# Performance work log

Measured on AMD Instinct MI355X. Metric: run time of the kernel, lower is better.

## Reference

```python
import jax, jax.numpy as jnp
import numpy as np

NUM_CLASSES = 1000
FEAT_DIM = 512
K = 2  # centers per class
BATCH = 32768


def setup_inputs() -> dict:
    key = jax.random.key(0)
    k1, k2, k3 = jax.random.split(key, 3)
    x = jax.random.normal(k1, (BATCH, FEAT_DIM), dtype=jnp.float32)
    labels = jax.random.randint(k2, (BATCH,), 0, NUM_CLASSES, dtype=jnp.int64)
    centers = jax.random.normal(k3, (NUM_CLASSES * K, FEAT_DIM), dtype=jnp.float32)
    return {"x": x, "labels": labels, "centers": centers}


def reference(x, labels, centers):
    # centers viewed as [num_classes, K, D]; gather per-sample class centers -> [B, K, D]
    c = centers.reshape(NUM_CLASSES, K, FEAT_DIM)[labels]
    # squared euclidean distance to each of the K centers, then min over K
    d = jnp.sum((x[:, None, :] - c) ** 2, axis=-1)  # [B, K]
    min_d = jnp.min(d, axis=-1)                      # [B]
    return jnp.mean(min_d)
```

## Files before the change

kernel.cpp:

```cpp
#include <hip/hip_runtime.h>

#define BATCH 32768
#define FEAT 512
#define KCENT 2

__global__ __launch_bounds__(256) void mcl_partial(
    const float* __restrict__ x,
    const int* __restrict__ labels,
    const float* __restrict__ centers,
    float* __restrict__ partial)
{
    const int wave = threadIdx.x >> 6;
    const int lane = threadIdx.x & 63;
    const int sample = blockIdx.x * 4 + wave;

    const int lab = labels[sample];
    const float* __restrict__ xrow = x + (size_t)sample * FEAT;
    const float* __restrict__ c0 = centers + (size_t)lab * (KCENT * FEAT);
    const float* __restrict__ c1 = c0 + FEAT;

    float d0 = 0.f, d1 = 0.f;
#pragma unroll
    for (int j = 0; j < 2; ++j) {
        const int off = j * 256 + lane * 4;
        const float4 xv = *(const float4*)(xrow + off);
        const float4 a  = *(const float4*)(c0 + off);
        const float4 b  = *(const float4*)(c1 + off);
        float e;
        e = xv.x - a.x; d0 += e * e;
        e = xv.y - a.y; d0 += e * e;
        e = xv.z - a.z; d0 += e * e;
        e = xv.w - a.w; d0 += e * e;
        e = xv.x - b.x; d1 += e * e;
        e = xv.y - b.y; d1 += e * e;
        e = xv.z - b.z; d1 += e * e;
        e = xv.w - b.w; d1 += e * e;
    }

#pragma unroll
    for (int s = 32; s > 0; s >>= 1) {
        d0 += __shfl_down(d0, s, 64);
        d1 += __shfl_down(d1, s, 64);
    }

    __shared__ float smin[4];
    if (lane == 0) smin[wave] = fminf(d0, d1);
    __syncthreads();
    if (threadIdx.x == 0)
        partial[blockIdx.x] = (smin[0] + smin[1]) + (smin[2] + smin[3]);
}

__global__ __launch_bounds__(256) void mcl_final(
    const float* __restrict__ partial, int n, float* __restrict__ out)
{
    float s = 0.f;
    for (int i = threadIdx.x; i < n; i += 256) s += partial[i];
#pragma unroll
    for (int sh = 32; sh > 0; sh >>= 1) s += __shfl_down(s, sh, 64);
    __shared__ float ws[4];
    const int wave = threadIdx.x >> 6;
    const int lane = threadIdx.x & 63;
    if (lane == 0) ws[wave] = s;
    __syncthreads();
    if (threadIdx.x == 0)
        out[0] = ((ws[0] + ws[1]) + (ws[2] + ws[3])) * (1.0f / (float)BATCH);
}

extern "C" void kernel_launch(void* const* d_in, const int* in_sizes, int n_in,
                              void* d_out, int out_size, void* d_ws, size_t ws_size,
                              hipStream_t stream) {
    const float* x       = (const float*)d_in[0];
    const int*   labels  = (const int*)d_in[1];
    const float* centers = (const float*)d_in[2];
    float* out = (float*)d_out;
    float* partial = (float*)d_ws;

    const int nblocks = BATCH / 4;
    mcl_partial<<<nblocks, 256, 0, stream>>>(x, labels, centers, partial);
    mcl_final<<<1, 256, 0, stream>>>(partial, nblocks, out);
}
```

Before: 108.2 us.

## Process four samples per wave with nontemporal x loads and fewer blocks

Each wave now handles four samples instead of one. Labels are loaded once per wave and broadcast by shuffle, the x rows are read with nontemporal loads, and the grid shrinks fourfold so the final reduction sums fewer partials with a compile-time trip count. The aim is to cut block launch and reduction overhead and keep the streamed x data from polluting cache used by the centers. In exchange, each wave serialises four reductions, which may lower memory-level parallelism unless the compiler overlaps the unrolled loads.

New measurement: 109.0 us. About the same (+0.8%).

```diff
diff --git a/kernel.cpp b/kernel.cpp
--- a/kernel.cpp
+++ b/kernel.cpp
@@ -3,6 +3,10 @@
 #define BATCH 32768
 #define FEAT 512
 #define KCENT 2
+#define SAMPLES_PER_WAVE 4
+#define NBLOCKS (BATCH / (4 * SAMPLES_PER_WAVE))
+
+typedef float vf4 __attribute__((ext_vector_type(4)));
 
 __global__ __launch_bounds__(256) void mcl_partial(
     const float* __restrict__ x,
@@ -12,49 +16,59 @@
 {
     const int wave = threadIdx.x >> 6;
     const int lane = threadIdx.x & 63;
-    const int sample = blockIdx.x * 4 + wave;
+    const int gw   = blockIdx.x * 4 + wave;
+    const int base = gw * SAMPLES_PER_WAVE;
 
-    const int lab = labels[sample];
-    const float* __restrict__ xrow = x + (size_t)sample * FEAT;
-    const float* __restrict__ c0 = centers + (size_t)lab * (KCENT * FEAT);
-    const float* __restrict__ c1 = c0 + FEAT;
+    int labv = 0;
+    if (lane < SAMPLES_PER_WAVE) labv = labels[base + lane];
 
-    float d0 = 0.f, d1 = 0.f;
+    float wsum = 0.f;
+
 #pragma unroll
-    for (int j = 0; j < 2; ++j) {
-        const int off = j * 256 + lane * 4;
-        const float4 xv = *(const float4*)(xrow + off);
-        const float4 a  = *(const float4*)(c0 + off);
-        const float4 b  = *(const float4*)(c1 + off);
-        float e;
-        e = xv.x - a.x; d0 += e * e;
-        e = xv.y - a.y; d0 += e * e;
-        e = xv.z - a.z; d0 += e * e;
-        e = xv.w - a.w; d0 += e * e;
-        e = xv.x - b.x; d1 += e * e;
-        e = xv.y - b.y; d1 += e * e;
-        e = xv.z - b.z; d1 += e * e;
-        e = xv.w - b.w; d1 += e * e;
+    for (int s = 0; s < SAMPLES_PER_WAVE; ++s) {
+        const int lab = __shfl(labv, s, 64);
+        const float* __restrict__ xrow = x + (size_t)(base + s) * FEAT;
+        const float* __restrict__ c0   = centers + (size_t)lab * (KCENT * FEAT);
+
+        float d0 = 0.f, d1 = 0.f;
+#pragma unroll
+        for (int j = 0; j < 2; ++j) {
+            const int off = j * 256 + lane * 4;
+            const vf4 xv = __builtin_nontemporal_load((const vf4*)(xrow + off));
+            const vf4 a  = *(const vf4*)(c0 + off);
+            const vf4 b  = *(const vf4*)(c0 + FEAT + off);
+            float e;
+            e = xv.x - a.x; d0 += e * e;
+            e = xv.y - a.y; d0 += e * e;
+            e = xv.z - a.z; d0 += e * e;
+            e = xv.w - a.w; d0 += e * e;
+            e = xv.x - b.x; d1 += e * e;
+            e = xv.y - b.y; d1 += e * e;
+            e = xv.z - b.z; d1 += e * e;
+            e = xv.w - b.w; d1 += e * e;
+        }
+
+#pragma unroll
+        for (int sh = 32; sh > 0; sh >>= 1) {
+            d0 += __shfl_down(d0, sh, 64);
+            d1 += __shfl_down(d1, sh, 64);
+        }
+        if (lane == 0) wsum += fminf(d0, d1);
     }
 
-#pragma unroll
-    for (int s = 32; s > 0; s >>= 1) {
-        d0 += __shfl_down(d0, s, 64);
-        d1 += __shfl_down(d1, s, 64);
-    }
-
-    __shared__ float smin[4];
-    if (lane == 0) smin[wave] = fminf(d0, d1);
+    __shared__ float sacc[4];
+    if (lane == 0) sacc[wave] = wsum;
     __syncthreads();
     if (threadIdx.x == 0)
-        partial[blockIdx.x] = (smin[0] + smin[1]) + (smin[2] + smin[3]);
+        partial[blockIdx.x] = (sacc[0] + sacc[1]) + (sacc[2] + sacc[3]);
 }
 
 __global__ __launch_bounds__(256) void mcl_final(
     const float* __restrict__ partial, int n, float* __restrict__ out)
 {
     float s = 0.f;
-    for (int i = threadIdx.x; i < n; i += 256) s += partial[i];
+#pragma unroll
+    for (int i = threadIdx.x; i < NBLOCKS; i += 256) s += partial[i];
 #pragma unroll
     for (int sh = 32; sh > 0; sh >>= 1) s += __shfl_down(s, sh, 64);
     __shared__ float ws[4];
@@ -75,7 +89,6 @@
     float* out = (float*)d_out;
     float* partial = (float*)d_ws;
 
-    const int nblocks = BATCH / 4;
-    mcl_partial<<<nblocks, 256, 0, stream>>>(x, labels, centers, partial);
-    mcl_final<<<1, 256, 0, stream>>>(partial, nblocks, out);
+    mcl_partial<<<NBLOCKS, 256, 0, stream>>>(x, labels, centers, partial);
+    mcl_final<<<1, 256, 0, stream>>>(partial, NBLOCKS, out);
 }
```
